# Kernel optimization log

Measured on AMD Instinct MI355X. Metric: run time of the kernel, lower is better.

Reference implementation:

```python
import jax, jax.numpy as jnp
import numpy as np
import math

B, T, C, H = 8, 1024, 768, 12
HD = C // H  # 64


def setup_inputs() -> dict:
    key = jax.random.key(0)
    k1, k2, k3 = jax.random.split(key, 3)
    x = jax.random.normal(k1, (B, T, C), dtype=jnp.float32)
    W_attn = jax.random.normal(k2, (C, 3 * C), dtype=jnp.float32) * 0.02
    b_attn = jnp.zeros((3 * C,), dtype=jnp.float32)
    W_proj = jax.random.normal(k3, (C, C), dtype=jnp.float32) * (0.02 / math.sqrt(2 * 12))
    b_proj = jnp.zeros((C,), dtype=jnp.float32)
    return {"x": x, "W_attn": W_attn, "b_attn": b_attn, "W_proj": W_proj, "b_proj": b_proj}


def reference(x, W_attn, b_attn, W_proj, b_proj):
    Bx, Tx, Cx = x.shape
    qkv = x @ W_attn + b_attn                        # [B,T,3C]
    # faithful to original: reshape to (B,T,H,3*HD) then split last axis
    qkv = qkv.reshape(Bx, Tx, H, 3 * HD).transpose(0, 2, 1, 3)  # [B,H,T,3*HD]
    q, k, v = jnp.split(qkv, 3, axis=-1)             # each [B,H,T,HD]
    att = jnp.einsum('bhqd,bhkd->bhqk', q, k) / math.sqrt(HD)
    causal = jnp.tril(jnp.ones((Tx, Tx), dtype=bool))
    att = jnp.where(causal, att, -jnp.inf)
    att = jax.nn.softmax(att, axis=-1)
    y = jnp.einsum('bhqk,bhkd->bhqd', att, v)        # [B,H,T,HD]
    y = y.transpose(0, 2, 1, 3).reshape(Bx, Tx, Cx)  # [B,T,C]
    return y @ W_proj + b_proj
```

## Files before the change

### kernel.cpp

```cpp
#include <hip/hip_runtime.h>
#include <hip/hip_bf16.h>


#define TDIM 1024
#define CDIM 768
#define NDIM 2304

typedef __attribute__((ext_vector_type(8))) short bf16x8;
typedef __attribute__((ext_vector_type(8))) unsigned short u16x8;
typedef __attribute__((ext_vector_type(4))) float f32x4;

__device__ __forceinline__ unsigned short f2bf(float f) {
    unsigned int u;
    __builtin_memcpy(&u, &f, 4);
    u += 0x7FFFu + ((u >> 16) & 1u);
    return (unsigned short)(u >> 16);
}

__device__ __forceinline__ void async_copy16(void* lds, const void* g) {
    __builtin_amdgcn_global_load_lds(
        (const __attribute__((address_space(1))) void*)g,
        (__attribute__((address_space(3))) void*)lds, 16, 0, 0);
}

__global__ __launch_bounds__(256) void cast_x(const float* __restrict__ x,
                                              unsigned short* __restrict__ xb) {
    const size_t i = ((size_t)blockIdx.x * 256 + threadIdx.x) * 4;
    float4 v = *(const float4*)&x[i];
    ushort4 s;
    s.x = f2bf(v.x); s.y = f2bf(v.y); s.z = f2bf(v.z); s.w = f2bf(v.w);
    *(ushort4*)&xb[i] = s;
}

template <int N>
__global__ __launch_bounds__(256) void transpose_cast(const float* __restrict__ W,
                                                      unsigned short* __restrict__ Wt) {
    __shared__ float tile[32][33];
    const int n0 = blockIdx.x * 32;
    const int k0 = blockIdx.y * 32;
    const int tx = threadIdx.x & 31;
    const int ty = threadIdx.x >> 5;
#pragma unroll
    for (int i = 0; i < 4; ++i)
        tile[ty + i * 8][tx] = W[(size_t)(k0 + ty + i * 8) * N + n0 + tx];
    __syncthreads();
#pragma unroll
    for (int i = 0; i < 4; ++i)
        Wt[(size_t)(n0 + ty + i * 8) * CDIM + k0 + tx] = f2bf(tile[tx][ty + i * 8]);
}

__global__ __launch_bounds__(512, 4) void qkv_mfma(
    const unsigned short* __restrict__ xb, const unsigned short* __restrict__ Wt,
    const float* __restrict__ bias,
    unsigned short* __restrict__ Q, unsigned short* __restrict__ Kd,
    unsigned short* __restrict__ Vt)
{
    const int wg = ((int)blockIdx.x & 7) * 72 + ((int)blockIdx.x >> 3);
    const int bx = wg % 9;
    const int by = wg / 9;
    const int n0 = bx * 256;
    const int m0 = by * 128;
    const int tid = threadIdx.x;
    const int lane = tid & 63;
    const int w = tid >> 6;
    const int wm = w >> 2;
    const int wn = w & 3;
    const int lm = lane & 15;
    const int lq = lane >> 4;

    __shared__ __align__(16) unsigned short lds[36864];

    float bb[4];
#pragma unroll
    for (int ni = 0; ni < 4; ++ni) bb[ni] = bias[n0 + wn * 64 + ni * 16 + lm];

    f32x4 acc[4][4] = {};

    const int eo = lq ^ ((lm >> 1) & 3);
    int aoffc[4], boffc[4];
#pragma unroll
    for (int mi = 0; mi < 4; ++mi)
        aoffc[mi] = (wm * 64 + mi * 16 + lm) * 32 + eo * 8;
#pragma unroll
    for (int ni = 0; ni < 4; ++ni)
        boffc[ni] = 4096 + (wn * 64 + ni * 16 + lm) * 32 + eo * 8;

    const int rowA = tid >> 2;
    const int ccA = (tid & 3) ^ ((rowA >> 1) & 3);
    const int srcA = rowA * CDIM + ccA * 8;
    int srcB[2];
#pragma unroll
    for (int j = 0; j < 2; ++j) {
        const int lin = j * 512 + tid;
        const int rowB = lin >> 2;
        const int ccB = (lin & 3) ^ ((rowB >> 1) & 3);
        srcB[j] = rowB * CDIM + ccB * 8;
    }
    const unsigned short* xbb = xb + (size_t)m0 * CDIM;
    const unsigned short* Wtb = Wt + (size_t)n0 * CDIM;

#define STAGE(p, kt)                                                            \
    do {                                                                        \
        async_copy16(&lds[(p) * 12288 + w * 512], &xbb[srcA + (kt) * 32]);      \
        _Pragma("unroll")                                                       \
        for (int j = 0; j < 2; ++j)                                             \
            async_copy16(&lds[(p) * 12288 + 4096 + j * 4096 + w * 512],         \
                         &Wtb[srcB[j] + (kt) * 32]);                            \
    } while (0)

#define TILE(p, ktn)                                                            \
    do {                                                                        \
        STAGE((p + 2) % 3, ktn);                                                \
        bf16x8 a[4], b[4];                                                      \
        _Pragma("unroll")                                                       \
        for (int mi = 0; mi < 4; ++mi)                                          \
            a[mi] = *(const bf16x8*)&lds[(p) * 12288 + aoffc[mi]];              \
        _Pragma("unroll")                                                       \
        for (int ni = 0; ni < 4; ++ni)                                          \
            b[ni] = *(const bf16x8*)&lds[(p) * 12288 + boffc[ni]];              \
        __builtin_amdgcn_s_setprio(1);                                          \
        _Pragma("unroll")                                                       \
        for (int mi = 0; mi < 4; ++mi)                                          \
            _Pragma("unroll")                                                   \
            for (int ni = 0; ni < 4; ++ni)                                      \
                acc[mi][ni] = __builtin_amdgcn_mfma_f32_16x16x32_bf16(          \
                    a[mi], b[ni], acc[mi][ni], 0, 0, 0);                        \
        __builtin_amdgcn_s_setprio(0);                                          \
        asm volatile("s_waitcnt vmcnt(3)" ::: "memory");                        \
        __builtin_amdgcn_s_barrier();                                           \
    } while (0)

    STAGE(0, 0);
    STAGE(1, 1);
    asm volatile("s_waitcnt vmcnt(3)" ::: "memory");
    __builtin_amdgcn_s_barrier();

#pragma unroll 1
    for (int it = 0; it < 8; ++it) {
        const int k2 = (3 * it + 2 < 24) ? 3 * it + 2 : 23;
        const int k3 = (3 * it + 3 < 24) ? 3 * it + 3 : 23;
        const int k4 = (3 * it + 4 < 24) ? 3 * it + 4 : 23;
        TILE(0, k2);
        TILE(1, k3);
        TILE(2, k4);
    }

#undef STAGE
#undef TILE

    asm volatile("s_waitcnt vmcnt(0)" ::: "memory");
    __builtin_amdgcn_s_barrier();

    const int ga = bx * 4 + wn;
    const int which = ga % 3;
    const int h = ga / 3;

    if (which == 2) {
#pragma unroll
        for (int ni = 0; ni < 4; ++ni) {
            const int d = ni * 16 + lm;
#pragma unroll
            for (int mi = 0; mi < 4; ++mi) {
                const int gm0 = m0 + wm * 64 + mi * 16 + lq * 4;
                const int bidx = gm0 >> 10;
                const int t0 = gm0 & 1023;
                ushort4 sv;
                sv.x = f2bf(acc[mi][ni][0] + bb[ni]);
                sv.y = f2bf(acc[mi][ni][1] + bb[ni]);
                sv.z = f2bf(acc[mi][ni][2] + bb[ni]);
                sv.w = f2bf(acc[mi][ni][3] + bb[ni]);
                *(ushort4*)&Vt[(((size_t)bidx * 12 + h) * 64 + d) * TDIM + t0] = sv;
            }
        }
    } else {
        unsigned short* dst = (which == 0) ? Q : Kd;
        unsigned short* Es = &lds[w * 1152];
        const int erow = lane >> 2;
        const int ecol = lane & 3;
#pragma unroll
        for (int mi = 0; mi < 4; ++mi) {
#pragma unroll
            for (int r = 0; r < 4; ++r)
#pragma unroll
                for (int ni = 0; ni < 4; ++ni)
                    Es[(lq * 4 + r) * 72 + ni * 16 + lm] = f2bf(acc[mi][ni][r] + bb[ni]);
            const int t = m0 + wm * 64 + mi * 16 + erow;
            const int bidx = t >> 10;
            const int tt = t & 1023;
            unsigned short* drow = &dst[(((size_t)bidx * 12 + h) * TDIM + tt) * 64];
            u16x8 v0 = *(const u16x8*)&Es[erow * 72 + ecol * 16];
            u16x8 v1 = *(const u16x8*)&Es[erow * 72 + ecol * 16 + 8];
            *(u16x8*)&drow[ecol * 16] = v0;
            *(u16x8*)&drow[ecol * 16 + 8] = v1;
        }
    }
}

#define ATTN_TILE(aq, q0t, qt_t, l_p, o, ksb, vsb) do {                         \
    const bool diag_ = (kt == (qt_t));                                          \
    float pf[4][4];                                                             \
    _Pragma("unroll")                                                           \
    for (int nt = 0; nt < 4; ++nt) {                                            \
        f32x4 s = {};                                                           \
        _Pragma("unroll")                                                       \
        for (int kc = 0; kc < 2; ++kc) {                                        \
            bf16x8 bfrag = *(const bf16x8*)&(ksb)[(nt * 16 + lm) * 64 + cofs[kc]]; \
            s = __builtin_amdgcn_mfma_f32_16x16x32_bf16(aq[kc], bfrag, s, 0, 0, 0); \
        }                                                                       \
        const int keyg = kbase + nt * 16 + lm;                                  \
        _Pragma("unroll")                                                       \
        for (int r = 0; r < 4; ++r) {                                           \
            float p = __builtin_amdgcn_exp2f(s[r] * SC);                        \
            if (diag_) {                                                        \
                const int qg = (q0t) + w * 16 + lq * 4 + r;                     \
                if (keyg > qg) p = 0.f;                                         \
            }                                                                   \
            pf[nt][r] = p;                                                      \
        }                                                                       \
    }                                                                           \
    _Pragma("unroll")                                                           \
    for (int r = 0; r < 4; ++r) {                                               \
        l_p[r] += pf[0][r] + pf[1][r] + pf[2][r] + pf[3][r];                    \
        _Pragma("unroll")                                                       \
        for (int nt = 0; nt < 4; ++nt)                                          \
            Ps[w][lq * 4 + r][nt * 16 + lm] = f2bf(pf[nt][r]);                  \
    }                                                                           \
    {                                                                           \
        bf16x8 ap[2];                                                           \
        _Pragma("unroll")                                                       \
        for (int kc = 0; kc < 2; ++kc)                                          \
            ap[kc] = *(const bf16x8*)&Ps[w][lm][kc * 32 + lq * 8];              \
        _Pragma("unroll")                                                       \
        for (int nt = 0; nt < 4; ++nt) {                                        \
            _Pragma("unroll")                                                   \
            for (int kc = 0; kc < 2; ++kc) {                                    \
                bf16x8 bv = *(const bf16x8*)&(vsb)[(nt * 16 + lm) * 64 + cofs[kc]]; \
                o[nt] = __builtin_amdgcn_mfma_f32_16x16x32_bf16(ap[kc], bv, o[nt], 0, 0, 0); \
            }                                                                   \
        }                                                                       \
    }                                                                           \
} while (0)

#define ATTN_EPI(q0t, l_p, o) do {                                              \
    _Pragma("unroll")                                                           \
    for (int r = 0; r < 4; ++r) {                                               \
        float l = l_p[r];                                                       \
        _Pragma("unroll")                                                       \
        for (int off = 1; off < 16; off <<= 1) l += __shfl_xor(l, off);         \
        const float inv = 1.0f / l;                                             \
        const int qg = (q0t) + w * 16 + lq * 4 + r;                             \
        _Pragma("unroll")                                                       \
        for (int nt = 0; nt < 4; ++nt)                                          \
            Yb[(size_t)qg * 64 + nt * 16 + lm] = f2bf(o[nt][r] * inv);          \
    }                                                                           \
} while (0)

__global__ __launch_bounds__(256) void attn_mfma(
    const unsigned short* __restrict__ Q, const unsigned short* __restrict__ K,
    const unsigned short* __restrict__ Vt, unsigned short* __restrict__ Y)
{
    const int pi = blockIdx.x;
    const int bh = blockIdx.y;
    const int qtA = pi, qtB = 15 - pi;
    const int q0A = qtA * 64, q0B = qtB * 64;
    const int tid = threadIdx.x;
    const int lane = tid & 63;
    const int w = tid >> 6;
    const int lm = lane & 15;
    const int lq = lane >> 4;

    __shared__ __align__(16) unsigned short Ks2[2][4096];
    __shared__ __align__(16) unsigned short Vts2[2][4096];
    __shared__ __align__(16) unsigned short Ps[4][16][72];

    const unsigned short* Qb = Q + (size_t)bh * TDIM * 64;
    const unsigned short* Kb = K + (size_t)bh * TDIM * 64;
    const unsigned short* Vtb = Vt + (size_t)bh * 64 * TDIM;
    unsigned short* Yb = Y + (size_t)bh * TDIM * 64;

    bf16x8 aqA[2], aqB[2];
#pragma unroll
    for (int kc = 0; kc < 2; ++kc) {
        aqA[kc] = *(const bf16x8*)&Qb[(size_t)(q0A + w * 16 + lm) * 64 + kc * 32 + lq * 8];
        aqB[kc] = *(const bf16x8*)&Qb[(size_t)(q0B + w * 16 + lm) * 64 + kc * 32 + lq * 8];
    }

    int dstO[2], srcK[2], srcV[2];
#pragma unroll
    for (int it = 0; it < 2; ++it) {
        const int idx = it * 256 + tid;
        const int row = idx >> 3;
        const int cc = (idx & 7) ^ (row & 7);
        dstO[it] = idx * 8;
        srcK[it] = row * 64 + cc * 8;
        srcV[it] = row * TDIM + cc * 8;
    }
    int cofs[2];
#pragma unroll
    for (int kc = 0; kc < 2; ++kc)
        cofs[kc] = (((kc * 4 + lq) ^ (lm & 7)) * 8);

#define AST(bf, kb)                                                             \
    do {                                                                        \
        _Pragma("unroll")                                                       \
        for (int it = 0; it < 2; ++it) {                                        \
            async_copy16(&Ks2[bf][dstO[it]], &Kb[(size_t)(kb) * 64 + srcK[it]]); \
            async_copy16(&Vts2[bf][dstO[it]], &Vtb[(size_t)(kb) + srcV[it]]);   \
        }                                                                       \
    } while (0)

    float lA[4] = {}, lB[4] = {};
    f32x4 oA[4] = {}, oB[4] = {};

    const float SC = 0.125f * 1.44269504f;
    const int nktA = qtA + 1;
    const int nktB = qtB + 1;

    int buf = 0;
    AST(0, 0);
    asm volatile("s_waitcnt vmcnt(0)" ::: "memory");
    __builtin_amdgcn_s_barrier();

    for (int kt = 0; kt < nktB; ++kt) {
        const int kbase = kt * 64;
        if (kt + 1 < nktB) AST(buf ^ 1, kbase + 64);

        ATTN_TILE(aqB, q0B, qtB, lB, oB, Ks2[buf], Vts2[buf]);
        if (kt < nktA) ATTN_TILE(aqA, q0A, qtA, lA, oA, Ks2[buf], Vts2[buf]);

        asm volatile("s_waitcnt vmcnt(0)" ::: "memory");
        __builtin_amdgcn_s_barrier();
        buf ^= 1;
    }

#undef AST

    ATTN_EPI(q0A, lA, oA);
    ATTN_EPI(q0B, lB, oB);
}

__global__ __launch_bounds__(256) void proj_mfma(
    const unsigned short* __restrict__ Y, const unsigned short* __restrict__ Wt,
    const float* __restrict__ bias, float* __restrict__ out)
{
    const int n0 = blockIdx.x * 128;
    const int m0 = blockIdx.y * 128;
    const int tid = threadIdx.x;
    const int lane = tid & 63;
    const int w = tid >> 6;
    const int wm = w & 1;
    const int wn = w >> 1;
    const int lm = lane & 15;
    const int lq = lane >> 4;

    __shared__ __align__(16) unsigned short As[128 * 32];
    __shared__ __align__(16) unsigned short Bs[128 * 32];

    f32x4 acc[4][4] = {};

    const int srow = lane >> 2;
    const int schunk = lane & 3;

    for (int k0 = 0; k0 < CDIM; k0 += 32) {
        const int h = k0 >> 6;
        const int inner = k0 & 63;
        __syncthreads();
#pragma unroll
        for (int c = 0; c < 2; ++c) {
            const int rbase = c * 64 + w * 16;
            const int m = m0 + rbase + srow;
            const int bidx = m >> 10;
            const int t = m & 1023;
            async_copy16(&As[rbase * 32],
                         &Y[(((size_t)bidx * 12 + h) * TDIM + t) * 64 + inner + schunk * 8]);
            async_copy16(&Bs[rbase * 32],
                         &Wt[(size_t)(n0 + rbase + srow) * CDIM + k0 + schunk * 8]);
        }
        __syncthreads();

        bf16x8 a[4], b[4];
#pragma unroll
        for (int mi = 0; mi < 4; ++mi)
            a[mi] = *(const bf16x8*)&As[(wm * 64 + mi * 16 + lm) * 32 + lq * 8];
#pragma unroll
        for (int ni = 0; ni < 4; ++ni)
            b[ni] = *(const bf16x8*)&Bs[(wn * 64 + ni * 16 + lm) * 32 + lq * 8];
#pragma unroll
        for (int mi = 0; mi < 4; ++mi)
#pragma unroll
            for (int ni = 0; ni < 4; ++ni)
                acc[mi][ni] = __builtin_amdgcn_mfma_f32_16x16x32_bf16(
                    a[mi], b[ni], acc[mi][ni], 0, 0, 0);
    }

#pragma unroll
    for (int ni = 0; ni < 4; ++ni) {
        const int gn = n0 + wn * 64 + ni * 16 + lm;
        const float bb = bias[gn];
#pragma unroll
        for (int mi = 0; mi < 4; ++mi) {
#pragma unroll
            for (int r = 0; r < 4; ++r) {
                const int gm = m0 + wm * 64 + mi * 16 + lq * 4 + r;
                out[(size_t)gm * CDIM + gn] = acc[mi][ni][r] + bb;
            }
        }
    }
}

extern "C" void kernel_launch(void* const* d_in, const int* in_sizes, int n_in,
                              void* d_out, int out_size, void* d_ws, size_t ws_size,
                              hipStream_t stream) {
    const float* x      = (const float*)d_in[0];
    const float* W_attn = (const float*)d_in[1];
    const float* b_attn = (const float*)d_in[2];
    const float* W_proj = (const float*)d_in[3];
    const float* b_proj = (const float*)d_in[4];
    float* out = (float*)d_out;

    const size_t per = (size_t)8 * 12 * 1024 * 64;
    unsigned short* Q   = (unsigned short*)d_ws;
    unsigned short* K   = Q + per;
    unsigned short* Vt  = K + per;
    unsigned short* xb  = Vt + per;
    unsigned short* Wta = xb + (size_t)8192 * CDIM;
    unsigned short* Wtp = Wta + (size_t)NDIM * CDIM;

    cast_x<<<dim3(6144), 256, 0, stream>>>(x, xb);
    transpose_cast<NDIM><<<dim3(72, 24), 256, 0, stream>>>(W_attn, Wta);
    transpose_cast<CDIM><<<dim3(24, 24), 256, 0, stream>>>(W_proj, Wtp);

    qkv_mfma<<<dim3(576), 512, 0, stream>>>(xb, Wta, b_attn, Q, K, Vt);
    attn_mfma<<<dim3(8, 96), 256, 0, stream>>>(Q, K, Vt, Q);
    proj_mfma<<<dim3(6, 64), 256, 0, stream>>>(Q, Wtp, b_proj, out);
}
```

Before: 187.5 us.

## Fuse precast kernels and triple-buffer the projection GEMM with swizzled LDS

Merges the x cast and both weight transpose-casts into one launch, which removes two kernel launches. Rewrites the output-projection GEMM to use a three-stage async global-to-LDS pipeline with a single barrier per k-step. It also adds an XOR swizzle on LDS chunks to cut bank conflicts, XCD-aware block remapping, hoisted bias loads and MFMA priority hints. These additions bring more LDS use and register pressure (launch bounds 256,3) and more complex wait counting.

```diff
diff --git a/kernel.cpp b/kernel.cpp
--- a/kernel.cpp
+++ b/kernel.cpp
@@ -23,23 +23,37 @@
         (__attribute__((address_space(3))) void*)lds, 16, 0, 0);
 }
 
-__global__ __launch_bounds__(256) void cast_x(const float* __restrict__ x,
-                                              unsigned short* __restrict__ xb) {
-    const size_t i = ((size_t)blockIdx.x * 256 + threadIdx.x) * 4;
-    float4 v = *(const float4*)&x[i];
-    ushort4 s;
-    s.x = f2bf(v.x); s.y = f2bf(v.y); s.z = f2bf(v.z); s.w = f2bf(v.w);
-    *(ushort4*)&xb[i] = s;
-}
-
-template <int N>
-__global__ __launch_bounds__(256) void transpose_cast(const float* __restrict__ W,
-                                                      unsigned short* __restrict__ Wt) {
+__global__ __launch_bounds__(256) void precast(
+    const float* __restrict__ x, unsigned short* __restrict__ xb,
+    const float* __restrict__ Wa, unsigned short* __restrict__ Wta,
+    const float* __restrict__ Wp, unsigned short* __restrict__ Wtp)
+{
     __shared__ float tile[32][33];
-    const int n0 = blockIdx.x * 32;
-    const int k0 = blockIdx.y * 32;
-    const int tx = threadIdx.x & 31;
-    const int ty = threadIdx.x >> 5;
+    int bid = blockIdx.x;
+    const int tid = threadIdx.x;
+
+    if (bid < 6144) {
+        const size_t i = ((size_t)bid * 256 + tid) * 4;
+        float4 v = *(const float4*)&x[i];
+        ushort4 s;
+        s.x = f2bf(v.x); s.y = f2bf(v.y); s.z = f2bf(v.z); s.w = f2bf(v.w);
+        *(ushort4*)&xb[i] = s;
+        return;
+    }
+    bid -= 6144;
+    const float* W;
+    unsigned short* Wt;
+    int N, bx, by;
+    if (bid < 1728) {
+        W = Wa; Wt = Wta; N = NDIM; bx = bid % 72; by = bid / 72;
+    } else {
+        bid -= 1728;
+        W = Wp; Wt = Wtp; N = CDIM; bx = bid % 24; by = bid / 24;
+    }
+    const int n0 = bx * 32;
+    const int k0 = by * 32;
+    const int tx = tid & 31;
+    const int ty = tid >> 5;
 #pragma unroll
     for (int i = 0; i < 4; ++i)
         tile[ty + i * 8][tx] = W[(size_t)(k0 + ty + i * 8) * N + n0 + tx];
@@ -339,70 +353,117 @@
     ATTN_EPI(q0B, lB, oB);
 }
 
-__global__ __launch_bounds__(256) void proj_mfma(
+__global__ __launch_bounds__(256, 3) void proj_mfma(
     const unsigned short* __restrict__ Y, const unsigned short* __restrict__ Wt,
     const float* __restrict__ bias, float* __restrict__ out)
 {
-    const int n0 = blockIdx.x * 128;
-    const int m0 = blockIdx.y * 128;
+    const int wg = ((int)blockIdx.x & 7) * 48 + ((int)blockIdx.x >> 3);
+    const int bx = wg % 6;
+    const int by = wg / 6;
+    const int n0 = bx * 128;
+    const int m0 = by * 128;
     const int tid = threadIdx.x;
     const int lane = tid & 63;
     const int w = tid >> 6;
-    const int wm = w & 1;
-    const int wn = w >> 1;
+    const int wm = w >> 1;
+    const int wn = w & 1;
     const int lm = lane & 15;
     const int lq = lane >> 4;
 
-    __shared__ __align__(16) unsigned short As[128 * 32];
-    __shared__ __align__(16) unsigned short Bs[128 * 32];
+    __shared__ __align__(16) unsigned short lds[24576];
+
+    float bb[4];
+#pragma unroll
+    for (int ni = 0; ni < 4; ++ni) bb[ni] = bias[n0 + wn * 64 + ni * 16 + lm];
 
     f32x4 acc[4][4] = {};
 
-    const int srow = lane >> 2;
-    const int schunk = lane & 3;
-
-    for (int k0 = 0; k0 < CDIM; k0 += 32) {
-        const int h = k0 >> 6;
-        const int inner = k0 & 63;
-        __syncthreads();
-#pragma unroll
-        for (int c = 0; c < 2; ++c) {
-            const int rbase = c * 64 + w * 16;
-            const int m = m0 + rbase + srow;
-            const int bidx = m >> 10;
-            const int t = m & 1023;
-            async_copy16(&As[rbase * 32],
-                         &Y[(((size_t)bidx * 12 + h) * TDIM + t) * 64 + inner + schunk * 8]);
-            async_copy16(&Bs[rbase * 32],
-                         &Wt[(size_t)(n0 + rbase + srow) * CDIM + k0 + schunk * 8]);
-        }
-        __syncthreads();
-
-        bf16x8 a[4], b[4];
-#pragma unroll
-        for (int mi = 0; mi < 4; ++mi)
-            a[mi] = *(const bf16x8*)&As[(wm * 64 + mi * 16 + lm) * 32 + lq * 8];
-#pragma unroll
-        for (int ni = 0; ni < 4; ++ni)
-            b[ni] = *(const bf16x8*)&Bs[(wn * 64 + ni * 16 + lm) * 32 + lq * 8];
-#pragma unroll
-        for (int mi = 0; mi < 4; ++mi)
-#pragma unroll
-            for (int ni = 0; ni < 4; ++ni)
-                acc[mi][ni] = __builtin_amdgcn_mfma_f32_16x16x32_bf16(
-                    a[mi], b[ni], acc[mi][ni], 0, 0, 0);
-    }
+    const int eo = lq ^ ((lm >> 1) & 3);
+    int aoffc[4], boffc[4];
+#pragma unroll
+    for (int mi = 0; mi < 4; ++mi)
+        aoffc[mi] = (wm * 64 + mi * 16 + lm) * 32 + eo * 8;
+#pragma unroll
+    for (int ni = 0; ni < 4; ++ni)
+        boffc[ni] = 4096 + (wn * 64 + ni * 16 + lm) * 32 + eo * 8;
+
+    size_t srcA[2];
+    int srcB[2];
+#pragma unroll
+    for (int j = 0; j < 2; ++j) {
+        const int lin = j * 256 + tid;
+        const int row = lin >> 2;
+        const int cc = (lin & 3) ^ ((row >> 1) & 3);
+        const int m = m0 + row;
+        srcA[j] = (size_t)(m >> 10) * 786432 + (size_t)(m & 1023) * 64 + cc * 8;
+        srcB[j] = row * CDIM + cc * 8;
+    }
+    const unsigned short* Wtb = Wt + (size_t)n0 * CDIM;
+
+#define PSTAGE(p, kt)                                                           \
+    do {                                                                        \
+        const int hof = ((kt) >> 1) * 65536 + ((kt) & 1) * 32;                  \
+        _Pragma("unroll")                                                       \
+        for (int j = 0; j < 2; ++j)                                             \
+            async_copy16(&lds[(p) * 8192 + (j * 256 + tid) * 8],                \
+                         &Y[srcA[j] + hof]);                                    \
+        _Pragma("unroll")                                                       \
+        for (int j = 0; j < 2; ++j)                                             \
+            async_copy16(&lds[(p) * 8192 + 4096 + (j * 256 + tid) * 8],         \
+                         &Wtb[srcB[j] + (kt) * 32]);                            \
+    } while (0)
+
+#define PTILE(p, ktn)                                                           \
+    do {                                                                        \
+        PSTAGE((p + 2) % 3, ktn);                                               \
+        bf16x8 a[4], b[4];                                                      \
+        _Pragma("unroll")                                                       \
+        for (int mi = 0; mi < 4; ++mi)                                          \
+            a[mi] = *(const bf16x8*)&lds[(p) * 8192 + aoffc[mi]];               \
+        _Pragma("unroll")                                                       \
+        for (int ni = 0; ni < 4; ++ni)                                          \
+            b[ni] = *(const bf16x8*)&lds[(p) * 8192 + boffc[ni]];               \
+        __builtin_amdgcn_s_setprio(1);                                          \
+        _Pragma("unroll")                                                       \
+        for (int mi = 0; mi < 4; ++mi)                                          \
+            _Pragma("unroll")                                                   \
+            for (int ni = 0; ni < 4; ++ni)                                      \
+                acc[mi][ni] = __builtin_amdgcn_mfma_f32_16x16x32_bf16(          \
+                    a[mi], b[ni], acc[mi][ni], 0, 0, 0);                        \
+        __builtin_amdgcn_s_setprio(0);                                          \
+        asm volatile("s_waitcnt vmcnt(4)" ::: "memory");                        \
+        __builtin_amdgcn_s_barrier();                                           \
+    } while (0)
+
+    PSTAGE(0, 0);
+    PSTAGE(1, 1);
+    asm volatile("s_waitcnt vmcnt(4)" ::: "memory");
+    __builtin_amdgcn_s_barrier();
+
+#pragma unroll 1
+    for (int it = 0; it < 8; ++it) {
+        const int k2 = (3 * it + 2 < 24) ? 3 * it + 2 : 23;
+        const int k3 = (3 * it + 3 < 24) ? 3 * it + 3 : 23;
+        const int k4 = (3 * it + 4 < 24) ? 3 * it + 4 : 23;
+        PTILE(0, k2);
+        PTILE(1, k3);
+        PTILE(2, k4);
+    }
+
+#undef PSTAGE
+#undef PTILE
+
+    asm volatile("s_waitcnt vmcnt(0)" ::: "memory");
 
 #pragma unroll
     for (int ni = 0; ni < 4; ++ni) {
         const int gn = n0 + wn * 64 + ni * 16 + lm;
-        const float bb = bias[gn];
 #pragma unroll
         for (int mi = 0; mi < 4; ++mi) {
 #pragma unroll
             for (int r = 0; r < 4; ++r) {
                 const int gm = m0 + wm * 64 + mi * 16 + lq * 4 + r;
-                out[(size_t)gm * CDIM + gn] = acc[mi][ni][r] + bb;
+                out[(size_t)gm * CDIM + gn] = acc[mi][ni][r] + bb[ni];
             }
         }
     }
@@ -426,11 +487,9 @@
     unsigned short* Wta = xb + (size_t)8192 * CDIM;
     unsigned short* Wtp = Wta + (size_t)NDIM * CDIM;
 
-    cast_x<<<dim3(6144), 256, 0, stream>>>(x, xb);
-    transpose_cast<NDIM><<<dim3(72, 24), 256, 0, stream>>>(W_attn, Wta);
-    transpose_cast<CDIM><<<dim3(24, 24), 256, 0, stream>>>(W_proj, Wtp);
+    precast<<<dim3(8448), 256, 0, stream>>>(x, xb, W_attn, Wta, W_proj, Wtp);
 
     qkv_mfma<<<dim3(576), 512, 0, stream>>>(xb, Wta, b_attn, Q, K, Vt);
     attn_mfma<<<dim3(8, 96), 256, 0, stream>>>(Q, K, Vt, Q);
-    proj_mfma<<<dim3(6, 64), 256, 0, stream>>>(Q, Wtp, b_proj, out);
-}
+    proj_mfma<<<dim3(384), 256, 0, stream>>>(Q, Wtp, b_proj, out);
+}
```

Measured after the change: 182.1 us, median of 2. -2.9%, faster.
